# Kernel optimization log

Hardware: AMD Instinct MI355X
Metric: run time of the kernel (lower is better)

The kernel has to match this reference:

```python
import jax, jax.numpy as jnp
import numpy as np
import math

D_MODEL = 512
H = 8
N_LAYERS = 4
D_FF = 2048
HEAD_DIM = D_MODEL // H


def setup_inputs() -> dict:
    key = jax.random.key(0)
    ks = jax.random.split(key, 12)
    s = 1.0 / math.sqrt(D_MODEL)
    x = jax.random.normal(ks[0], (16, 1024, D_MODEL), dtype=jnp.float32)
    # shared head module (same weights for all H heads, per original ModuleList aliasing)
    wq = jax.random.normal(ks[1], (D_MODEL, HEAD_DIM), dtype=jnp.float32) * s
    bq = jnp.zeros((HEAD_DIM,), dtype=jnp.float32)
    wk = jax.random.normal(ks[2], (D_MODEL, HEAD_DIM), dtype=jnp.float32) * s
    bk = jnp.zeros((HEAD_DIM,), dtype=jnp.float32)
    wv = jax.random.normal(ks[3], (D_MODEL, HEAD_DIM), dtype=jnp.float32) * s
    bv = jnp.zeros((HEAD_DIM,), dtype=jnp.float32)
    wo = jax.random.normal(ks[4], (D_MODEL, D_MODEL), dtype=jnp.float32) * s
    bo = jnp.zeros((D_MODEL,), dtype=jnp.float32)
    # shared LayerNorm params (one LN instance used everywhere)
    ln_g = jnp.ones((D_MODEL,), dtype=jnp.float32)
    ln_b = jnp.zeros((D_MODEL,), dtype=jnp.float32)
    w1 = jax.random.normal(ks[5], (D_MODEL, D_FF), dtype=jnp.float32) * s
    b1 = jnp.zeros((D_FF,), dtype=jnp.float32)
    w2 = jax.random.normal(ks[6], (D_FF, D_MODEL), dtype=jnp.float32) * (1.0 / math.sqrt(D_FF))
    b2 = jnp.zeros((D_MODEL,), dtype=jnp.float32)
    return {"x": x, "wq": wq, "bq": bq, "wk": wk, "bk": bk, "wv": wv, "bv": bv,
            "wo": wo, "bo": bo, "ln_g": ln_g, "ln_b": ln_b,
            "w1": w1, "b1": b1, "w2": w2, "b2": b2}


def _layernorm(x, g, b, eps=1e-5):
    mu = jnp.mean(x, axis=-1, keepdims=True)
    var = jnp.var(x, axis=-1, keepdims=True)
    return (x - mu) * jax.lax.rsqrt(var + eps) * g + b


def _mha(x, wq, bq, wk, bk, wv, bv, wo, bo):
    # All H heads share identical weights, so compute one head and tile the concat.
    q = x @ wq + bq                      # [b, s, hd]
    k = x @ wk + bk                      # [b, s, hd]
    v = x @ wv + bv                      # [b, s, hd]
    scores = jnp.einsum('bqd,bkd->bqk', q, k) / math.sqrt(D_MODEL / H)
    # NOTE: original applies Softmax(dim=1) on a [b, s_q, s_k] tensor -> softmax over q axis
    attn = jax.nn.softmax(scores, axis=1)
    head = jnp.einsum('bqk,bkd->bqd', attn, v)   # [b, s, hd]
    concat = jnp.tile(head, (1, 1, H))           # [b, s, d_model] (H identical heads)
    return concat @ wo + bo


def reference(x, wq, bq, wk, bk, wv, bv, wo, bo, ln_g, ln_b, w1, b1, w2, b2):
    for _ in range(N_LAYERS):
        attn = _mha(x, wq, bq, wk, bk, wv, bv, wo, bo)
        h = _layernorm(attn + x, ln_g, ln_b)
        ff = (jnp.maximum(h @ w1 + b1, 0.0) if False else (h @ w1 + b1)) @ w2 + b2  # no relu in original forward
        x = _layernorm(h + ff, ln_g, ln_b)
    return x
```

## Files before the change

### kernel.cpp

```cpp
#include <hip/hip_runtime.h>
#include <hip/hip_bf16.h>

#define DEV __device__ __forceinline__

typedef __bf16 bf16;
typedef __attribute__((ext_vector_type(8))) __bf16 bf16x8;
typedef __attribute__((ext_vector_type(4))) __bf16 bf16x4;
typedef __attribute__((ext_vector_type(4))) float f32x4;

static constexpr int B = 16, S = 1024, D = 512, HD = 64, FF = 2048;
static constexpr int BS = B * S;
static constexpr int QKVLD = 192;

typedef const __attribute__((address_space(1))) void gas_void;
typedef __attribute__((address_space(3))) void las_void;

DEV void gload16(const void* g, void* l) {
  __builtin_amdgcn_global_load_lds((gas_void*)g, (las_void*)l, 16, 0, 0);
}

DEV void store_out(float* p, float v) { *p = v; }
DEV void store_out(bf16* p, float v) { *p = (bf16)v; }

#define MEMFENCE asm volatile("" ::: "memory")
#define VMCNT(n) asm volatile("s_waitcnt vmcnt(" #n ")" ::: "memory")

template<int BM, typename OutT>
__global__ __launch_bounds__(512, 1) void k_gemm8p(
    const bf16* __restrict__ A, const bf16* __restrict__ Bt, OutT* __restrict__ C,
    int K, int lda, int ldb, int ldc, int gn, float alpha, const float* __restrict__ bias)
{
  static_assert(BM == 128 || BM == 256, "");
  constexpr int HM = BM / 2;
  constexpr int FMH = HM / 2 / 16;
  constexpr int GL_A = HM / 64;
  constexpr int GL_B = 2;

  __shared__ bf16 sA[2][2][HM * 64];
  __shared__ bf16 sB[2][2][128 * 64];

  const int tid = threadIdx.x;
  const int lane = tid & 63;
  const int wid = tid >> 6;
  const int wm = wid >> 2;
  const int wn = wid & 3;
  const int lr = lane & 15;
  const int lk8 = (lane >> 4) * 8;

  const int nwg = gridDim.x;
  const int bid = blockIdx.x;
  const int swz = (bid & 7) * (nwg >> 3) + (bid >> 3);
  const int im = swz / gn, in = swz % gn;
  const int bm0 = im * BM, bn0 = in * 256;

  A += (long)bm0 * lda;
  Bt += (long)bn0 * ldb;

  const int NT = K >> 6;
  const int NI = NT >> 1;

  auto stageA = [&](int buf, int h, int t) {
    if (t >= NT) return;
    const bf16* src = A + (long)t * 64;
#pragma unroll
    for (int it = 0; it < GL_A; ++it) {
      int c = it * 512 + tid;
      int row = c >> 3;
      int cc = (c & 7) ^ (row & 7);
      gload16(src + (long)(h * HM + row) * lda + cc * 8, &sA[buf][h][c * 8]);
    }
  };
  auto stageB = [&](int buf, int h, int t) {
    if (t >= NT) return;
    const bf16* src = Bt + (long)t * 64;
#pragma unroll
    for (int it = 0; it < GL_B; ++it) {
      int c = it * 512 + tid;
      int row = c >> 3;
      int cc = (c & 7) ^ (row & 7);
      gload16(src + (long)(h * 128 + row) * ldb + cc * 8, &sB[buf][h][c * 8]);
    }
  };

  f32x4 acc[4][FMH * 2] = {};

  stageA(0, 0, 0); stageB(0, 1, 0); stageA(0, 1, 0); stageB(0, 0, 0);
  stageA(1, 0, 1); stageB(1, 1, 1);
  if (GL_A == 2) { VMCNT(4); } else { VMCNT(3); }
  MEMFENCE; __builtin_amdgcn_s_barrier(); MEMFENCE;

#define PHASE(b, qm, qn, STAGE, ...) do {                                        \
    bf16x8 af[FMH][2], bg[2][2];                                                 \
    _Pragma("unroll") for (int fm = 0; fm < FMH; ++fm)                           \
    _Pragma("unroll") for (int kx = 0; kx < 2; ++kx) {                           \
      int ra = wm * (HM / 2) + fm * 16 + lr;                                     \
      int e = kx * 32 + lk8;                                                     \
      af[fm][kx] = *(const bf16x8*)((const char*)&sA[b][qm][0] +                 \
                     (ra * 8 + ((e >> 3) ^ (ra & 7))) * 16);                     \
    }                                                                            \
    _Pragma("unroll") for (int fn = 0; fn < 2; ++fn)                             \
    _Pragma("unroll") for (int kx = 0; kx < 2; ++kx) {                           \
      int rb = wn * 32 + fn * 16 + lr;                                           \
      int e = kx * 32 + lk8;                                                     \
      bg[fn][kx] = *(const bf16x8*)((const char*)&sB[b][qn][0] +                 \
                     (rb * 8 + ((e >> 3) ^ (rb & 7))) * 16);                     \
    }                                                                            \
    STAGE;                                                                       \
    MEMFENCE; __builtin_amdgcn_s_barrier(); MEMFENCE;                            \
    __builtin_amdgcn_s_setprio(1);                                               \
    _Pragma("unroll") for (int kx = 0; kx < 2; ++kx)                             \
    _Pragma("unroll") for (int fm = 0; fm < FMH; ++fm)                           \
    _Pragma("unroll") for (int fn = 0; fn < 2; ++fn)                             \
      acc[qm * 2 + qn][fm * 2 + fn] = __builtin_amdgcn_mfma_f32_16x16x32_bf16(   \
          af[fm][kx], bg[fn][kx], acc[qm * 2 + qn][fm * 2 + fn], 0, 0, 0);       \
    __builtin_amdgcn_s_setprio(0);                                               \
    __VA_ARGS__;                                                                 \
    MEMFENCE; __builtin_amdgcn_s_barrier(); MEMFENCE;                            \
  } while (0)

  for (int i = 0; i < NI; ++i) {
    const int t1 = 2 * i + 1, t2 = 2 * i + 2, t3 = 2 * i + 3;
    const bool more = (t2 < NT);
    PHASE(0, 0, 0, stageA(1, 1, t1));
    PHASE(0, 0, 1, stageB(1, 0, t1));
    PHASE(0, 1, 1, stageA(0, 0, t2));
    PHASE(0, 1, 0, stageB(0, 1, t2),
          if (more) { if (GL_A == 2) { VMCNT(4); } else { VMCNT(3); } }
          else { VMCNT(0); });
    PHASE(1, 0, 0, stageA(0, 1, t2));
    PHASE(1, 0, 1, stageB(0, 0, t2));
    PHASE(1, 1, 1, stageA(1, 0, t3));
    PHASE(1, 1, 0, stageB(1, 1, t3),
          if (more) { if (GL_A == 2) { VMCNT(4); } else { VMCNT(3); } });
  }
#undef PHASE

  const int r0 = (lane >> 4) * 4;
#pragma unroll
  for (int qm = 0; qm < 2; ++qm)
#pragma unroll
  for (int qn = 0; qn < 2; ++qn)
#pragma unroll
  for (int fm = 0; fm < FMH; ++fm)
#pragma unroll
  for (int fn = 0; fn < 2; ++fn) {
    int gc = bn0 + qn * 128 + wn * 32 + fn * 16 + lr;
    float bv = bias ? bias[gc] : 0.f;
#pragma unroll
    for (int r = 0; r < 4; ++r) {
      int gr = bm0 + qm * HM + wm * (HM / 2) + fm * 16 + r0 + r;
      store_out(C + (long)gr * ldc + gc, acc[qm * 2 + qn][fm * 2 + fn][r] * alpha + bv);
    }
  }
}

template<int NT, bool DB>
__global__ __launch_bounds__(512, 2) void k_gemm_ln(
    const bf16* __restrict__ A, const bf16* __restrict__ Bt,
    const float* __restrict__ resid, const float* __restrict__ bias,
    const float* __restrict__ g, const float* __restrict__ be,
    float* __restrict__ fo, bf16* __restrict__ bo16)
{
  constexpr int K = NT * 64;
  constexpr int NB = DB ? 2 : 1;
  __shared__ bf16 sA[NB][64 * 64];
  __shared__ bf16 sB[NB][512 * 64];
  __shared__ float lsum[2][64][2];

  const int tid = threadIdx.x;
  const int lane = tid & 63;
  const int wid = tid >> 6;
  const int wm = wid >> 1;
  const int wn = wid & 1;
  const int lr = lane & 15;
  const int lk8 = (lane >> 4) * 8;
  const long bm0 = (long)blockIdx.x * 64;

  const bf16* Ab = A + bm0 * K;

  auto stage = [&](int buf, int t) {
    {
      int c = tid;
      int row = c >> 3;
      int cc = (c & 7) ^ (row & 7);
      gload16(Ab + (long)row * K + t * 64 + cc * 8, &sA[buf][c * 8]);
    }
#pragma unroll
    for (int it = 0; it < 8; ++it) {
      int c = it * 512 + tid;
      int row = c >> 3;
      int cc = (c & 7) ^ (row & 7);
      gload16(Bt + (long)row * K + t * 64 + cc * 8, &sB[buf][c * 8]);
    }
  };

  f32x4 acc[16] = {};
  auto compute = [&](int buf) {
#pragma unroll
    for (int kx = 0; kx < 2; ++kx) {
      int ra = wm * 16 + lr;
      int ech = (kx * 32 + lk8) >> 3;
      bf16x8 af = *(const bf16x8*)((const char*)&sA[buf][0] +
                    (ra * 8 + (ech ^ (ra & 7))) * 16);
#pragma unroll
      for (int fn = 0; fn < 16; ++fn) {
        int rb = wn * 256 + fn * 16 + lr;
        bf16x8 bg = *(const bf16x8*)((const char*)&sB[buf][0] +
                      (rb * 8 + (ech ^ (rb & 7))) * 16);
        acc[fn] = __builtin_amdgcn_mfma_f32_16x16x32_bf16(af, bg, acc[fn], 0, 0, 0);
      }
    }
  };

  stage(0, 0);
  VMCNT(0); MEMFENCE;
  __syncthreads();
  if constexpr (DB) {
    for (int t = 0; t < NT; ++t) {
      if (t + 1 < NT) stage((t & 1) ^ 1, t + 1);
      compute(t & 1);
      VMCNT(0); MEMFENCE;
      __syncthreads();
    }
  } else {
    compute(0);
  }

  const int r0 = (lane >> 4) * 4;
  float s[4] = {}, s2[4] = {};
#pragma unroll
  for (int fn = 0; fn < 16; ++fn) {
    int gc = wn * 256 + fn * 16 + lr;
    float bv = bias[gc];
#pragma unroll
    for (int r = 0; r < 4; ++r) {
      long gr = bm0 + wm * 16 + r0 + r;
      float y = acc[fn][r] + bv + resid[gr * 512 + gc];
      acc[fn][r] = y;
      s[r] += y; s2[r] += y * y;
    }
  }
#pragma unroll
  for (int m = 1; m < 16; m <<= 1)
#pragma unroll
    for (int r = 0; r < 4; ++r) { s[r] += __shfl_xor(s[r], m); s2[r] += __shfl_xor(s2[r], m); }
  if (lr == 0) {
#pragma unroll
    for (int r = 0; r < 4; ++r) {
      lsum[wn][wm * 16 + r0 + r][0] = s[r];
      lsum[wn][wm * 16 + r0 + r][1] = s2[r];
    }
  }
  __syncthreads();
  float mean[4], rstd[4];
#pragma unroll
  for (int r = 0; r < 4; ++r) {
    int row = wm * 16 + r0 + r;
    float S1 = lsum[0][row][0] + lsum[1][row][0];
    float S2 = lsum[0][row][1] + lsum[1][row][1];
    mean[r] = S1 * (1.f / 512);
    float var = S2 * (1.f / 512) - mean[r] * mean[r];
    rstd[r] = rsqrtf(var + 1e-5f);
  }
#pragma unroll
  for (int fn = 0; fn < 16; ++fn) {
    int gc = wn * 256 + fn * 16 + lr;
    float gv = g[gc], bev = be[gc];
#pragma unroll
    for (int r = 0; r < 4; ++r) {
      long gr = bm0 + wm * 16 + r0 + r;
      float yn = (acc[fn][r] - mean[r]) * rstd[r] * gv + bev;
      fo[gr * 512 + gc] = yn;
      bo16[gr * 512 + gc] = (bf16)yn;
    }
  }
}

template<int BM, int BN, int BK, int WM, int WN, typename OutT, bool EXPF>
__global__ __launch_bounds__(WM* WN * 64) void k_gemm(
    const bf16* __restrict__ A, const bf16* __restrict__ Bt, OutT* __restrict__ C,
    int K, int lda, int ldb, int ldc, float alpha, const float* __restrict__ bias,
    long aB, long bB, long cB)
{
  constexpr int NW = WM * WN;
  constexpr int T = NW * 64;
  constexpr int FM = BM / WM / 16;
  constexpr int FN = BN / WN / 16;
  constexpr int CPR = BK / 8;
  constexpr int CHA = BM * BK / 8;
  constexpr int CHB = BN * BK / 8;
  constexpr int IA = CHA / T;
  constexpr int IB = CHB / T;
  static_assert(CHA % T == 0 && CHB % T == 0, "staging divisibility");

  __shared__ bf16 sA[BM * BK];
  __shared__ bf16 sB[BN * BK];

  const int tid = threadIdx.x;
  const int lane = tid & 63;
  const int wid = tid >> 6;
  const int wm = wid / WN, wn = wid % WN;
  const int bm0 = blockIdx.x * BM;
  const int bn0 = blockIdx.y * BN;
  A += (long)blockIdx.z * aB + (long)bm0 * lda;
  Bt += (long)blockIdx.z * bB + (long)bn0 * ldb;
  C += (long)blockIdx.z * cB;

  f32x4 acc[FM][FN] = {};
  const int lr = lane & 15;
  const int lk = (lane >> 4) * 8;

  for (int k0 = 0; k0 < K; k0 += BK) {
#pragma unroll
    for (int i = 0; i < IA; ++i) {
      int c = i * T + tid;
      int row = c / CPR, kc = (c % CPR) * 8;
      gload16(A + (long)row * lda + k0 + kc, sA + c * 8);
    }
#pragma unroll
    for (int i = 0; i < IB; ++i) {
      int c = i * T + tid;
      int row = c / CPR, kc = (c % CPR) * 8;
      gload16(Bt + (long)row * ldb + k0 + kc, sB + c * 8);
    }
    asm volatile("s_waitcnt vmcnt(0)" ::: "memory");
    __syncthreads();

#pragma unroll
    for (int kk = 0; kk < BK; kk += 32) {
      bf16x8 af[FM], bg[FN];
#pragma unroll
      for (int m = 0; m < FM; ++m) {
        int row = wm * (FM * 16) + m * 16 + lr;
        af[m] = *(const bf16x8*)(sA + row * BK + kk + lk);
      }
#pragma unroll
      for (int n = 0; n < FN; ++n) {
        int col = wn * (FN * 16) + n * 16 + lr;
        bg[n] = *(const bf16x8*)(sB + col * BK + kk + lk);
      }
#pragma unroll
      for (int m = 0; m < FM; ++m)
#pragma unroll
        for (int n = 0; n < FN; ++n)
          acc[m][n] = __builtin_amdgcn_mfma_f32_16x16x32_bf16(af[m], bg[n], acc[m][n], 0, 0, 0);
    }
    __syncthreads();
  }

  const int r0 = (lane >> 4) * 4;
#pragma unroll
  for (int m = 0; m < FM; ++m) {
#pragma unroll
    for (int n = 0; n < FN; ++n) {
      int col = bn0 + wn * (FN * 16) + n * 16 + lr;
      float bv = bias ? bias[col] : 0.f;
#pragma unroll
      for (int r = 0; r < 4; ++r) {
        int row = bm0 + wm * (FM * 16) + m * 16 + r0 + r;
        float v = acc[m][n][r] * alpha + bv;
        if (EXPF) v = __expf(v);
        store_out(C + (long)row * ldc + col, v);
      }
    }
  }
}

__global__ __launch_bounds__(256) void k_cvt_dual(const float* __restrict__ in,
    float* __restrict__ fo, bf16* __restrict__ bo, long n4)
{
  long i = (long)blockIdx.x * 256 + threadIdx.x;
  if (i >= n4) return;
  float4 v = ((const float4*)in)[i];
  ((float4*)fo)[i] = v;
  bf16x4 h; h[0] = (bf16)v.x; h[1] = (bf16)v.y; h[2] = (bf16)v.z; h[3] = (bf16)v.w;
  ((bf16x4*)bo)[i] = h;
}

__global__ void k_tr(const float* __restrict__ in, bf16* __restrict__ out, int R, int C)
{
  __shared__ float t[32][33];
  int c0 = blockIdx.x * 32, r0 = blockIdx.y * 32;
#pragma unroll
  for (int i = 0; i < 4; ++i) {
    int r = r0 + threadIdx.y + i * 8;
    t[threadIdx.y + i * 8][threadIdx.x] = in[(long)r * C + c0 + threadIdx.x];
  }
  __syncthreads();
#pragma unroll
  for (int i = 0; i < 4; ++i) {
    int c = c0 + threadIdx.y + i * 8;
    out[(long)c * R + r0 + threadIdx.x] = (bf16)t[threadIdx.x][threadIdx.y + i * 8];
  }
}

__global__ __launch_bounds__(256) void k_woe(const float* __restrict__ wo, bf16* __restrict__ woet)
{
  int idx = blockIdx.x * 256 + threadIdx.x;
  int j = idx & 511, d = idx >> 9;
  float s = 0.f;
#pragma unroll
  for (int h = 0; h < 8; ++h) s += wo[(long)(h * 64 + d) * 512 + j];
  woet[(long)j * 64 + d] = (bf16)s;
}

__global__ void k_pack_bias(const float* __restrict__ bq, const float* __restrict__ bk,
                            const float* __restrict__ bv, float* __restrict__ o)
{
  int t = threadIdx.x;
  o[t] = bq[t]; o[64 + t] = bk[t]; o[128 + t] = bv[t];
}

__global__ __launch_bounds__(256) void k_colsum(const bf16* __restrict__ P, float* __restrict__ cs)
{
  int k = blockIdx.x * 256 + threadIdx.x;
  int b = blockIdx.y;
  const bf16* p = P + (long)b * S * S + k;
  float a0 = 0, a1 = 0, a2 = 0, a3 = 0;
  for (int q = 0; q < S; q += 4) {
    a0 += (float)p[(long)q * S];
    a1 += (float)p[(long)(q + 1) * S];
    a2 += (float)p[(long)(q + 2) * S];
    a3 += (float)p[(long)(q + 3) * S];
  }
  cs[b * S + k] = (a0 + a1) + (a2 + a3);
}

__global__ __launch_bounds__(256) void k_build_vnt(const bf16* __restrict__ qkv,
    const float* __restrict__ cs, bf16* __restrict__ vnt)
{
  int d = threadIdx.x & 63;
  int k = blockIdx.x * 4 + (threadIdx.x >> 6);
  int b = blockIdx.y;
  float v = (float)qkv[((long)(b * S + k)) * QKVLD + 128 + d];
  vnt[((long)b * HD + d) * S + k] = (bf16)(v / cs[b * S + k]);
}

extern "C" void kernel_launch(void* const* d_in, const int* in_sizes, int n_in,
                              void* d_out, int out_size, void* d_ws, size_t ws_size,
                              hipStream_t stream) {
  const float* x_in = (const float*)d_in[0];
  const float* wq = (const float*)d_in[1];
  const float* bq = (const float*)d_in[2];
  const float* wk = (const float*)d_in[3];
  const float* bk = (const float*)d_in[4];
  const float* wv = (const float*)d_in[5];
  const float* bv = (const float*)d_in[6];
  const float* wo = (const float*)d_in[7];
  const float* bo = (const float*)d_in[8];
  const float* ln_g = (const float*)d_in[9];
  const float* ln_b = (const float*)d_in[10];
  const float* w1 = (const float*)d_in[11];
  const float* b1 = (const float*)d_in[12];
  const float* w2 = (const float*)d_in[13];
  const float* b2 = (const float*)d_in[14];
  float* f_x = (float*)d_out;

  char* w = (char*)d_ws;
  size_t off = 0;
  auto alloc = [&](size_t bytes) { void* p = w + off; off += (bytes + 255) & ~(size_t)255; return p; };
  float* f_h   = (float*)alloc((size_t)BS * D * 4);
  bf16* b_x    = (bf16*)alloc((size_t)BS * D * 2);
  bf16* b_h    = (bf16*)alloc((size_t)BS * D * 2);
  bf16* b_qkv  = (bf16*)alloc((size_t)BS * QKVLD * 2);
  bf16* b_big  = (bf16*)alloc((size_t)BS * FF * 2);
  float* f_cs  = (float*)alloc((size_t)B * S * 4);
  bf16* b_vnt  = (bf16*)alloc((size_t)B * HD * S * 2);
  bf16* b_head = (bf16*)alloc((size_t)BS * HD * 2);
  bf16* wqkvT  = (bf16*)alloc((size_t)QKVLD * D * 2);
  bf16* woeT   = (bf16*)alloc((size_t)D * HD * 2);
  bf16* w1T    = (bf16*)alloc((size_t)FF * D * 2);
  bf16* w2T    = (bf16*)alloc((size_t)D * FF * 2);
  float* f_bqkv = (float*)alloc(192 * 4);

  k_cvt_dual<<<dim3(BS * D / 4 / 256), 256, 0, stream>>>(x_in, f_x, b_x, (long)BS * D / 4);
  k_tr<<<dim3(HD / 32, D / 32), dim3(32, 8), 0, stream>>>(wq, wqkvT, D, HD);
  k_tr<<<dim3(HD / 32, D / 32), dim3(32, 8), 0, stream>>>(wk, wqkvT + 64 * D, D, HD);
  k_tr<<<dim3(HD / 32, D / 32), dim3(32, 8), 0, stream>>>(wv, wqkvT + 128 * D, D, HD);
  k_tr<<<dim3(FF / 32, D / 32), dim3(32, 8), 0, stream>>>(w1, w1T, D, FF);
  k_tr<<<dim3(D / 32, FF / 32), dim3(32, 8), 0, stream>>>(w2, w2T, FF, D);
  k_woe<<<dim3(128), 256, 0, stream>>>(wo, woeT);
  k_pack_bias<<<1, 64, 0, stream>>>(bq, bk, bv, f_bqkv);

  for (int layer = 0; layer < 4; ++layer) {
    k_gemm<128, 64, 64, 4, 1, bf16, false><<<dim3(BS / 128, 3, 1), 256, 0, stream>>>(
        b_x, wqkvT, b_qkv, D, D, D, QKVLD, 1.f, f_bqkv, 0, 0, 0);
    k_gemm<128, 128, 64, 2, 2, bf16, true><<<dim3(S / 128, S / 128, B), 256, 0, stream>>>(
        b_qkv, b_qkv + 64, b_big, HD, QKVLD, QKVLD, S, 0.125f, nullptr,
        (long)S * QKVLD, (long)S * QKVLD, (long)S * S);
    k_colsum<<<dim3(S / 256, B), 256, 0, stream>>>(b_big, f_cs);
    k_build_vnt<<<dim3(S / 4, B), 256, 0, stream>>>(b_qkv, f_cs, b_vnt);
    k_gemm<64, 64, 64, 4, 1, bf16, false><<<dim3(S / 64, 1, B), 256, 0, stream>>>(
        b_big, b_vnt, b_head, S, S, S, HD, 1.f, nullptr,
        (long)S * S, (long)HD * S, (long)S * HD);
    k_gemm_ln<1, false><<<dim3(BS / 64), 512, 0, stream>>>(
        b_head, woeT, f_x, bo, ln_g, ln_b, f_h, b_h);
    k_gemm8p<256, bf16><<<dim3((BS / 256) * (FF / 256)), 512, 0, stream>>>(
        b_h, w1T, b_big, D, D, D, FF, FF / 256, 1.f, b1);
    k_gemm_ln<32, true><<<dim3(BS / 64), 512, 0, stream>>>(
        b_big, w2T, f_h, b2, ln_g, ln_b, f_x, b_x);
  }
}
```

Baseline: 980.7 us.

## Retile GEMM+LayerNorm warps to 64x64 and prefetch two K-stages ahead

Changes the k_gemm_ln warp layout from 4x2 (16 rows x 256 cols per warp) to 1x8 (all 64 rows x 64 cols per warp). Each warp now loads 4 A and 4 B fragments per k-step and reuses them across 16 MFMAs, which cuts redundant LDS reads of B. The pipeline also now issues two stages ahead with partial vmcnt waits, so global loads overlap compute across iterations. In exchange, the row-statistics reduction sums across 8 warps through a larger shared array, and each thread keeps more per-row state in registers.

```diff
diff --git a/kernel.cpp b/kernel.cpp
--- a/kernel.cpp
+++ b/kernel.cpp
@@ -154,7 +154,7 @@
   }
 }
 
-template<int NT, bool DB>
+template<int NT>
 __global__ __launch_bounds__(512, 2) void k_gemm_ln(
     const bf16* __restrict__ A, const bf16* __restrict__ Bt,
     const float* __restrict__ resid, const float* __restrict__ bias,
@@ -162,18 +162,16 @@
     float* __restrict__ fo, bf16* __restrict__ bo16)
 {
   constexpr int K = NT * 64;
-  constexpr int NB = DB ? 2 : 1;
+  constexpr int NB = (NT > 1) ? 2 : 1;
   __shared__ bf16 sA[NB][64 * 64];
   __shared__ bf16 sB[NB][512 * 64];
-  __shared__ float lsum[2][64][2];
+  __shared__ float lsum[8][64][2];
 
   const int tid = threadIdx.x;
   const int lane = tid & 63;
-  const int wid = tid >> 6;
-  const int wm = wid >> 1;
-  const int wn = wid & 1;
+  const int wn = tid >> 6;
   const int lr = lane & 15;
-  const int lk8 = (lane >> 4) * 8;
+  const int lkc = lane >> 4;
   const long bm0 = (long)blockIdx.x * 64;
 
   const bf16* Ab = A + bm0 * K;
@@ -194,85 +192,120 @@
     }
   };
 
-  f32x4 acc[16] = {};
+  f32x4 acc[4][4] = {};
   auto compute = [&](int buf) {
 #pragma unroll
     for (int kx = 0; kx < 2; ++kx) {
-      int ra = wm * 16 + lr;
-      int ech = (kx * 32 + lk8) >> 3;
-      bf16x8 af = *(const bf16x8*)((const char*)&sA[buf][0] +
-                    (ra * 8 + (ech ^ (ra & 7))) * 16);
-#pragma unroll
-      for (int fn = 0; fn < 16; ++fn) {
-        int rb = wn * 256 + fn * 16 + lr;
-        bf16x8 bg = *(const bf16x8*)((const char*)&sB[buf][0] +
-                      (rb * 8 + (ech ^ (rb & 7))) * 16);
-        acc[fn] = __builtin_amdgcn_mfma_f32_16x16x32_bf16(af, bg, acc[fn], 0, 0, 0);
-      }
+      bf16x8 af[4], bg[4];
+#pragma unroll
+      for (int fm = 0; fm < 4; ++fm) {
+        int ra = fm * 16 + lr;
+        int cc = (kx * 4 + lkc) ^ (ra & 7);
+        af[fm] = *(const bf16x8*)((const char*)&sA[buf][0] + ra * 128 + cc * 16);
+      }
+#pragma unroll
+      for (int fn = 0; fn < 4; ++fn) {
+        int rb = wn * 64 + fn * 16 + lr;
+        int cc = (kx * 4 + lkc) ^ (rb & 7);
+        bg[fn] = *(const bf16x8*)((const char*)&sB[buf][0] + rb * 128 + cc * 16);
+      }
+#pragma unroll
+      for (int fm = 0; fm < 4; ++fm)
+#pragma unroll
+        for (int fn = 0; fn < 4; ++fn)
+          acc[fm][fn] = __builtin_amdgcn_mfma_f32_16x16x32_bf16(af[fm], bg[fn], acc[fm][fn], 0, 0, 0);
     }
   };
 
-  stage(0, 0);
-  VMCNT(0); MEMFENCE;
+  if constexpr (NT == 1) {
+    stage(0, 0);
+    VMCNT(0); MEMFENCE;
+    __syncthreads();
+    compute(0);
+    __syncthreads();
+  } else {
+    stage(0, 0);
+    stage(1, 1);
+    VMCNT(9); MEMFENCE;
+    __syncthreads();
+    for (int t = 0; t < NT; ++t) {
+      compute(t & 1);
+      __syncthreads();
+      if (t + 2 < NT) {
+        stage(t & 1, t + 2);
+        VMCNT(9); MEMFENCE;
+      } else if (t + 1 < NT) {
+        VMCNT(0); MEMFENCE;
+      }
+      if (t + 1 < NT) __syncthreads();
+    }
+  }
+
+  float s[4][4], s2[4][4];
+#pragma unroll
+  for (int fm = 0; fm < 4; ++fm)
+#pragma unroll
+    for (int r = 0; r < 4; ++r) { s[fm][r] = 0.f; s2[fm][r] = 0.f; }
+
+#pragma unroll
+  for (int fn = 0; fn < 4; ++fn) {
+    int gc = wn * 64 + fn * 16 + lr;
+    float bv = bias[gc];
+#pragma unroll
+    for (int fm = 0; fm < 4; ++fm)
+#pragma unroll
+      for (int r = 0; r < 4; ++r) {
+        long gr = bm0 + fm * 16 + lkc * 4 + r;
+        float y = acc[fm][fn][r] + bv + resid[gr * 512 + gc];
+        acc[fm][fn][r] = y;
+        s[fm][r] += y; s2[fm][r] += y * y;
+      }
+  }
+#pragma unroll
+  for (int m = 1; m < 16; m <<= 1)
+#pragma unroll
+    for (int fm = 0; fm < 4; ++fm)
+#pragma unroll
+      for (int r = 0; r < 4; ++r) {
+        s[fm][r] += __shfl_xor(s[fm][r], m);
+        s2[fm][r] += __shfl_xor(s2[fm][r], m);
+      }
+  if (lr == 0) {
+#pragma unroll
+    for (int fm = 0; fm < 4; ++fm)
+#pragma unroll
+      for (int r = 0; r < 4; ++r) {
+        lsum[wn][fm * 16 + lkc * 4 + r][0] = s[fm][r];
+        lsum[wn][fm * 16 + lkc * 4 + r][1] = s2[fm][r];
+      }
+  }
   __syncthreads();
-  if constexpr (DB) {
-    for (int t = 0; t < NT; ++t) {
-      if (t + 1 < NT) stage((t & 1) ^ 1, t + 1);
-      compute(t & 1);
-      VMCNT(0); MEMFENCE;
-      __syncthreads();
-    }
-  } else {
-    compute(0);
-  }
-
-  const int r0 = (lane >> 4) * 4;
-  float s[4] = {}, s2[4] = {};
-#pragma unroll
-  for (int fn = 0; fn < 16; ++fn) {
-    int gc = wn * 256 + fn * 16 + lr;
-    float bv = bias[gc];
+  float mean[4][4], rstd[4][4];
+#pragma unroll
+  for (int fm = 0; fm < 4; ++fm)
 #pragma unroll
     for (int r = 0; r < 4; ++r) {
-      long gr = bm0 + wm * 16 + r0 + r;
-      float y = acc[fn][r] + bv + resid[gr * 512 + gc];
-      acc[fn][r] = y;
-      s[r] += y; s2[r] += y * y;
-    }
-  }
-#pragma unroll
-  for (int m = 1; m < 16; m <<= 1)
-#pragma unroll
-    for (int r = 0; r < 4; ++r) { s[r] += __shfl_xor(s[r], m); s2[r] += __shfl_xor(s2[r], m); }
-  if (lr == 0) {
-#pragma unroll
-    for (int r = 0; r < 4; ++r) {
-      lsum[wn][wm * 16 + r0 + r][0] = s[r];
-      lsum[wn][wm * 16 + r0 + r][1] = s2[r];
-    }
-  }
-  __syncthreads();
-  float mean[4], rstd[4];
-#pragma unroll
-  for (int r = 0; r < 4; ++r) {
-    int row = wm * 16 + r0 + r;
-    float S1 = lsum[0][row][0] + lsum[1][row][0];
-    float S2 = lsum[0][row][1] + lsum[1][row][1];
-    mean[r] = S1 * (1.f / 512);
-    float var = S2 * (1.f / 512) - mean[r] * mean[r];
-    rstd[r] = rsqrtf(var + 1e-5f);
-  }
-#pragma unroll
-  for (int fn = 0; fn < 16; ++fn) {
-    int gc = wn * 256 + fn * 16 + lr;
+      int row = fm * 16 + lkc * 4 + r;
+      float S1 = 0.f, S2 = 0.f;
+#pragma unroll
+      for (int w = 0; w < 8; ++w) { S1 += lsum[w][row][0]; S2 += lsum[w][row][1]; }
+      mean[fm][r] = S1 * (1.f / 512);
+      float var = S2 * (1.f / 512) - mean[fm][r] * mean[fm][r];
+      rstd[fm][r] = rsqrtf(var + 1e-5f);
+    }
+#pragma unroll
+  for (int fn = 0; fn < 4; ++fn) {
+    int gc = wn * 64 + fn * 16 + lr;
     float gv = g[gc], bev = be[gc];
 #pragma unroll
-    for (int r = 0; r < 4; ++r) {
-      long gr = bm0 + wm * 16 + r0 + r;
-      float yn = (acc[fn][r] - mean[r]) * rstd[r] * gv + bev;
-      fo[gr * 512 + gc] = yn;
-      bo16[gr * 512 + gc] = (bf16)yn;
-    }
+    for (int fm = 0; fm < 4; ++fm)
+#pragma unroll
+      for (int r = 0; r < 4; ++r) {
+        long gr = bm0 + fm * 16 + lkc * 4 + r;
+        float yn = (acc[fm][fn][r] - mean[fm][r]) * rstd[fm][r] * gv + bev;
+        fo[gr * 512 + gc] = yn;
+        bo16[gr * 512 + gc] = (bf16)yn;
+      }
   }
 }
 
@@ -493,11 +526,11 @@
     k_gemm<64, 64, 64, 4, 1, bf16, false><<<dim3(S / 64, 1, B), 256, 0, stream>>>(
         b_big, b_vnt, b_head, S, S, S, HD, 1.f, nullptr,
         (long)S * S, (long)HD * S, (long)S * HD);
-    k_gemm_ln<1, false><<<dim3(BS / 64), 512, 0, stream>>>(
+    k_gemm_ln<1><<<dim3(BS / 64), 512, 0, stream>>>(
         b_head, woeT, f_x, bo, ln_g, ln_b, f_h, b_h);
     k_gemm8p<256, bf16><<<dim3((BS / 256) * (FF / 256)), 512, 0, stream>>>(
         b_h, w1T, b_big, D, D, D, FF, FF / 256, 1.f, b1);
-    k_gemm_ln<32, true><<<dim3(BS / 64), 512, 0, stream>>>(
+    k_gemm_ln<32><<<dim3(BS / 64), 512, 0, stream>>>(
         b_big, w2T, f_h, b2, ln_g, ln_b, f_x, b_x);
   }
 }
```

Result: slower. 1.006 ms (+2.6%).
